# Kernel optimization log

Hardware: AMD Instinct MI355X
Metric: run time of the kernel (lower is better)

The kernel has to match this reference:

```python
import jax, jax.numpy as jnp
import numpy as np

EPS = 1e-6
D = 512      # embedding_dim
M = 4        # n_modules
B = 4        # batch
S = 128      # seq_len
K = 32       # stack_size
STEPS = 16   # max_steps (ACT)
SCALE = D ** (-0.5)


def _clin(zr, zi, Wr, Wi, sub):
    # complex linear: (Wr + i Wi)(zr + i zi), torch Linear convention y = x @ W.T
    yr = jnp.einsum(sub, zr, Wr) - jnp.einsum(sub, zi, Wi)
    yi = jnp.einsum(sub, zi, Wr) + jnp.einsum(sub, zr, Wi)
    return yr, yi


def forward_fn(x_real, x_imag, Wl_r, Wl_i, Wq_r, Wq_i, Wk_r, Wk_i, Wv_r, Wv_i,
               ln_scale, ln_shift, mod_bias, gate_mask,
               score_w, score_b, conf_w, conf_b, halt_w, halt_b,
               ctrl_w, ctrl_b, st_score_w, st_score_b, st_conf_w, st_conf_b):
    mem0 = jnp.zeros((B, K, 2 * D), x_real.dtype)
    ptr0 = jnp.zeros((B, K), x_real.dtype).at[:, 0].set(1.0)
    acc0 = jnp.zeros((B, S, 2 * D), x_real.dtype)
    rem0 = jnp.ones((B,), x_real.dtype)

    def step(carry, _):
        sr, si, mem, ptr, acc, rem = carry
        # ComplexAttentionBlock (all M modules vectorized on axis m)
        cr = 0.5 * x_real + 0.5 * sr
        ci = 0.5 * x_imag + 0.5 * si
        zr, zi = _clin(cr, ci, Wl_r, Wl_i, 'bsd,mod->bmso')   # [B,M,S,D]
        # ComplexLayerNorm (magnitude LN, unbiased var as torch.var default)
        mag = jnp.sqrt(zr * zr + zi * zi) + EPS
        mean = mag.mean(-1, keepdims=True)
        var = mag.var(-1, keepdims=True, ddof=1)
        nm = (mag - mean) / jnp.sqrt(var + EPS)
        nm = nm * ln_scale[None, :, None, :] + ln_shift[None, :, None, :]
        ph = jnp.arctan2(zi, zr)
        zr = nm * jnp.cos(ph)
        zi = nm * jnp.sin(ph)
        # ModReLU
        nrm = jnp.sqrt(zr * zr + zi * zi) + EPS
        sc = jax.nn.relu(nrm + mod_bias[None, :, None, :]) / nrm
        zr = zr * sc
        zi = zi * sc
        # ComplexAttention over concatenated real/imag q,k
        sub = 'bmsd,mod->bmso'
        qr, qi = _clin(zr, zi, Wq_r, Wq_i, sub)
        kr, ki = _clin(zr, zi, Wk_r, Wk_i, sub)
        vr, vi = _clin(zr, zi, Wv_r, Wv_i, sub)
        qf = jnp.concatenate([qr, qi], -1)   # [B,M,S,2D]
        kf = jnp.concatenate([kr, ki], -1)
        attn = jax.nn.softmax(jnp.einsum('bmse,bmte->bmst', qf, kf) * SCALE, axis=-1)
        ar = jnp.einsum('bmst,bmtd->bmsd', attn, vr)
        ai = jnp.einsum('bmst,bmtd->bmsd', attn, vi)
        # SigmoidGatingMask
        g = jax.nn.sigmoid(gate_mask)[None, :, None, :]
        pr = ar * g
        pi = ai * g
        flat = jnp.concatenate([pr, pi], -1)  # [B,M,S,2D]
        score = jnp.einsum('bmse,me->bms', flat, score_w) + score_b[None, :, None]
        conf = jax.nn.sigmoid(jnp.einsum('bmse,me->bms', flat, conf_w) + conf_b[None, :, None])
        halt = jnp.einsum('bmse,me->bms', flat, halt_w) + halt_b[None, :, None]
        # DifferentiableStack on seq-pooled broadcast state
        flat_in = jnp.concatenate([sr.mean(1), si.mean(1)], -1)  # [B,2D]
        control = jax.nn.softmax(flat_in @ ctrl_w + ctrl_b, axis=-1)  # [B,3]
        push, pop, noop = control[:, 0:1], control[:, 1:2], control[:, 2:3]
        ptr_up = jnp.roll(ptr, 1, axis=1)
        ptr_dn = jnp.roll(ptr, -1, axis=1)
        new_ptr = push * ptr_up + pop * ptr_dn + noop * ptr
        new_ptr = new_ptr / (new_ptr.sum(1, keepdims=True) + EPS)
        wmask = push * ptr_up                                   # [B,K]
        new_mem = wmask[..., None] * flat_in[:, None, :] + mem * (1.0 - wmask[..., None])
        read = (new_mem * new_ptr[..., None]).sum(1)            # [B,2D]
        sp_r, sp_i = read[:, :D], read[:, D:]
        st_sc = read @ st_score_w + st_score_b[0]               # [B]
        st_cf = jax.nn.sigmoid(read @ st_conf_w + st_conf_b[0])
        # combine M block proposals + stack proposal via score*confidence softmax
        all_pr = jnp.concatenate([pr, jnp.broadcast_to(sp_r[:, None, None, :], (B, 1, S, D))], 1)
        all_pi = jnp.concatenate([pi, jnp.broadcast_to(sp_i[:, None, None, :], (B, 1, S, D))], 1)
        all_sc = jnp.concatenate([score, jnp.broadcast_to(st_sc[:, None, None], (B, 1, S))], 1)
        all_cf = jnp.concatenate([conf, jnp.broadcast_to(st_cf[:, None, None], (B, 1, S))], 1)
        w = jax.nn.softmax(all_sc * all_cf, axis=1)[..., None]  # [B,M+1,S,1]
        new_sr = (w * all_pr).sum(1)
        new_si = (w * all_pi).sum(1)
        # ACT halting accumulation
        p = jax.nn.sigmoid(halt).mean(axis=(1, 2))              # [B]
        acc = acc + (p * rem)[:, None, None] * jnp.concatenate([new_sr, new_si], -1)
        rem = rem * (1.0 - p)
        return (new_sr, new_si, new_mem, new_ptr, acc, rem), None

    carry, _ = jax.lax.scan(step, (x_real, x_imag, mem0, ptr0, acc0, rem0), None, length=STEPS)
    sr, si, _, _, acc, rem = carry
    # add ACT remainder weight on final state
    out = acc + rem[:, None, None] * jnp.concatenate([sr, si], -1)
    return out  # [B,S,2D] real/imag concat


def setup_inputs() -> dict:
    key = jax.random.key(0)
    ks = jax.random.split(key, 24)
    w = 1.0 / np.sqrt(D)
    h = 0.02
    inp = {
        'x_real': jax.random.normal(ks[0], (B, S, D), jnp.float32),
        'x_imag': jax.random.normal(ks[1], (B, S, D), jnp.float32),
        'Wl_r': jax.random.normal(ks[2], (M, D, D), jnp.float32) * w,
        'Wl_i': jax.random.normal(ks[3], (M, D, D), jnp.float32) * w,
        'Wq_r': jax.random.normal(ks[4], (M, D, D), jnp.float32) * w,
        'Wq_i': jax.random.normal(ks[5], (M, D, D), jnp.float32) * w,
        'Wk_r': jax.random.normal(ks[6], (M, D, D), jnp.float32) * w,
        'Wk_i': jax.random.normal(ks[7], (M, D, D), jnp.float32) * w,
        'Wv_r': jax.random.normal(ks[8], (M, D, D), jnp.float32) * w,
        'Wv_i': jax.random.normal(ks[9], (M, D, D), jnp.float32) * w,
        'ln_scale': jnp.ones((M, D), jnp.float32),
        'ln_shift': jnp.zeros((M, D), jnp.float32),
        'mod_bias': jnp.zeros((M, D), jnp.float32),
        'gate_mask': jnp.ones((M, D), jnp.float32),
        'score_w': jax.random.normal(ks[10], (M, 2 * D), jnp.float32) * h,
        'score_b': jnp.zeros((M,), jnp.float32),
        'conf_w': jax.random.normal(ks[11], (M, 2 * D), jnp.float32) * h,
        'conf_b': jnp.zeros((M,), jnp.float32),
        'halt_w': jax.random.normal(ks[12], (M, 2 * D), jnp.float32) * h,
        'halt_b': jnp.full((M,), -4.0, jnp.float32),  # nn.init.constant_(halt_head.bias, -4.0)
        'ctrl_w': jax.random.normal(ks[13], (2 * D, 3), jnp.float32) * h,
        'ctrl_b': jnp.zeros((3,), jnp.float32),
        'st_score_w': jax.random.normal(ks[14], (2 * D,), jnp.float32) * h,
        'st_score_b': jnp.zeros((1,), jnp.float32),
        'st_conf_w': jax.random.normal(ks[15], (2 * D,), jnp.float32) * h,
        'st_conf_b': jnp.zeros((1,), jnp.float32),
    }
    return inp


def reference(x_real, x_imag, Wl_r, Wl_i, Wq_r, Wq_i, Wk_r, Wk_i, Wv_r, Wv_i,
              ln_scale, ln_shift, mod_bias, gate_mask,
              score_w, score_b, conf_w, conf_b, halt_w, halt_b,
              ctrl_w, ctrl_b, st_score_w, st_score_b, st_conf_w, st_conf_b):
    return forward_fn(x_real, x_imag, Wl_r, Wl_i, Wq_r, Wq_i, Wk_r, Wk_i, Wv_r, Wv_i,
                      ln_scale, ln_shift, mod_bias, gate_mask,
                      score_w, score_b, conf_w, conf_b, halt_w, halt_b,
                      ctrl_w, ctrl_b, st_score_w, st_score_b, st_conf_w, st_conf_b)
```

## Files before the change

kernel.cpp:

```cpp
#include <hip/hip_runtime.h>

#define DD 512
#define MM 4
#define BB 4
#define SS 128
#define KK 32
#define NSTEPS 16
#define EPSF 1e-6f
#define SCALEF 0.04419417382415922f

typedef unsigned short u16;
typedef __bf16 bf16x8 __attribute__((ext_vector_type(8)));
typedef u16 u16x8 __attribute__((ext_vector_type(8)));
typedef float f32x16 __attribute__((ext_vector_type(16)));

__device__ inline void split_bf16(float x, u16& h, u16& l) {
  __bf16 hb = (__bf16)x;
  float hf = (float)hb;
  __bf16 lb = (__bf16)(x - hf);
  h = __builtin_bit_cast(u16, hb);
  l = __builtin_bit_cast(u16, lb);
}

__global__ void k_convw(const float* __restrict__ src, u16* __restrict__ dst) {
  int idx = blockIdx.x * 256 + threadIdx.x;
  int row = idx >> 9, k = idx & 511;
  u16 h, l;
  split_bf16(src[idx], h, l);
  dst[(size_t)row * 1024 + k] = h;
  dst[(size_t)row * 1024 + 512 + k] = l;
}

__global__ void k_init(const float* __restrict__ xr, const float* __restrict__ xi,
                       float* __restrict__ sr, float* __restrict__ si,
                       float* __restrict__ acc, float* __restrict__ memv,
                       float* __restrict__ ptrv, float* __restrict__ rem,
                       u16* __restrict__ crbf, u16* __restrict__ cibf) {
  int idx = blockIdx.x * 256 + threadIdx.x;
  if (idx < BB * SS * 2 * DD) acc[idx] = 0.f;
  if (idx < BB * SS * DD) {
    float a = xr[idx], b = xi[idx];
    sr[idx] = a; si[idx] = b;
    int row = idx >> 9, d = idx & 511;
    u16 h, l;
    split_bf16(a, h, l);
    crbf[(size_t)row * 1024 + d] = h;
    crbf[(size_t)row * 1024 + 512 + d] = l;
    split_bf16(b, h, l);
    cibf[(size_t)row * 1024 + d] = h;
    cibf[(size_t)row * 1024 + 512 + d] = l;
  }
  if (idx < BB * KK * 2 * DD) memv[idx] = 0.f;
  if (idx < BB * KK) ptrv[idx] = ((idx & (KK - 1)) == 0) ? 1.f : 0.f;
  if (idx < BB) rem[idx] = 1.f;
}

__global__ void k_flatctrl(const float* __restrict__ sr, const float* __restrict__ si,
                           const float* __restrict__ ctrl_w, const float* __restrict__ ctrl_b,
                           float* __restrict__ ptrv, float* __restrict__ flat_in,
                           float* __restrict__ nptrg, float* __restrict__ wmg,
                           float* __restrict__ stacc) {
  int b = blockIdx.x;
  int tid = threadIdx.x;
  __shared__ float red[3 * 256];
  __shared__ float ctrl[3], optr[KK], nptr_s[KK], wm_s[KK], normf;

  if (tid < KK) optr[tid] = ptrv[b * KK + tid];

  int e4 = tid * 4;
  const float* basep = (e4 < DD) ? sr : si;
  int d4 = (e4 < DD) ? e4 : (e4 - DD);
  float4 accv = make_float4(0.f, 0.f, 0.f, 0.f);
  size_t base = (size_t)b * SS * DD + d4;
  for (int s = 0; s < SS; s++) {
    float4 v = *(const float4*)&basep[base + (size_t)s * DD];
    accv.x += v.x; accv.y += v.y; accv.z += v.z; accv.w += v.w;
  }
  accv.x *= (1.0f / SS); accv.y *= (1.0f / SS); accv.z *= (1.0f / SS); accv.w *= (1.0f / SS);
  *(float4*)&flat_in[b * 2 * DD + e4] = accv;
  float fv[4] = {accv.x, accv.y, accv.z, accv.w};
  float d0 = 0.f, d1 = 0.f, d2 = 0.f;
#pragma unroll
  for (int j = 0; j < 4; j++) {
    d0 += fv[j] * ctrl_w[(e4 + j) * 3 + 0];
    d1 += fv[j] * ctrl_w[(e4 + j) * 3 + 1];
    d2 += fv[j] * ctrl_w[(e4 + j) * 3 + 2];
  }
  red[tid] = d0; red[256 + tid] = d1; red[512 + tid] = d2;
  __syncthreads();
  for (int off = 128; off > 0; off >>= 1) {
    if (tid < off) {
      red[tid] += red[tid + off];
      red[256 + tid] += red[256 + tid + off];
      red[512 + tid] += red[512 + tid + off];
    }
    __syncthreads();
  }
  if (tid == 0) {
    float l0 = red[0] + ctrl_b[0], l1 = red[256] + ctrl_b[1], l2 = red[512] + ctrl_b[2];
    float mx = fmaxf(l0, fmaxf(l1, l2));
    float e0 = expf(l0 - mx), e1 = expf(l1 - mx), e2 = expf(l2 - mx);
    float s = e0 + e1 + e2;
    ctrl[0] = e0 / s; ctrl[1] = e1 / s; ctrl[2] = e2 / s;
    stacc[b * 2] = 0.f; stacc[b * 2 + 1] = 0.f;
  }
  __syncthreads();
  if (tid < KK) {
    float up = optr[(tid + KK - 1) & (KK - 1)];
    float dn = optr[(tid + 1) & (KK - 1)];
    float cu = optr[tid];
    nptr_s[tid] = ctrl[0] * up + ctrl[1] * dn + ctrl[2] * cu;
    wm_s[tid] = ctrl[0] * up;
  }
  __syncthreads();
  if (tid == 0) {
    float s = 0.f;
    for (int k = 0; k < KK; k++) s += nptr_s[k];
    normf = 1.f / (s + EPSF);
  }
  __syncthreads();
  if (tid < KK) {
    float np = nptr_s[tid] * normf;
    ptrv[b * KK + tid] = np;
    nptrg[b * KK + tid] = np;
    wmg[b * KK + tid] = wm_s[tid];
  }
}

#define LSTR 72

__global__ __launch_bounds__(256) void k_gemm_mfma(
    const u16* __restrict__ Ar, const u16* __restrict__ Ai,
    const u16* __restrict__ Wr, const u16* __restrict__ Wi,
    float* __restrict__ Cr, float* __restrict__ Ci) {
  __shared__ u16 sAr[64][LSTR], sAi[64][LSTR], sWr[64][LSTR], sWi[64][LSTR];
  int m = blockIdx.z;
  int row_blk = blockIdx.y * 64, o_blk = blockIdx.x * 64;
  int tid = threadIdx.x;

  int lrow = tid >> 3, lk8 = (tid & 7) << 3;
  size_t arow0 = (size_t)(row_blk + lrow), arow1 = arow0 + 32;
  size_t wrow0 = (size_t)m * DD + o_blk + lrow, wrow1 = wrow0 + 32;

  int wave = tid >> 6, lane = tid & 63;
  int wrow = (wave >> 1) * 32, wcol = (wave & 1) * 32;
  int l31 = lane & 31, khalf = (lane >> 5) * 8;

  f32x16 accP, accN, accI;
  for (int i = 0; i < 16; i++) { accP[i] = 0.f; accN[i] = 0.f; accI[i] = 0.f; }

  u16x8 g0 = *(const u16x8*)&Ar[arow0 * 1024 + lk8];
  u16x8 g1 = *(const u16x8*)&Ar[arow1 * 1024 + lk8];
  u16x8 g2 = *(const u16x8*)&Ai[arow0 * 1024 + lk8];
  u16x8 g3 = *(const u16x8*)&Ai[arow1 * 1024 + lk8];
  u16x8 g4 = *(const u16x8*)&Wr[wrow0 * 1024 + lk8];
  u16x8 g5 = *(const u16x8*)&Wr[wrow1 * 1024 + lk8];
  u16x8 g6 = *(const u16x8*)&Wi[wrow0 * 1024 + lk8];
  u16x8 g7 = *(const u16x8*)&Wi[wrow1 * 1024 + lk8];

  for (int it = 0; it < 24; ++it) {
    __syncthreads();
    *(u16x8*)&sAr[lrow][lk8] = g0;
    *(u16x8*)&sAr[lrow + 32][lk8] = g1;
    *(u16x8*)&sAi[lrow][lk8] = g2;
    *(u16x8*)&sAi[lrow + 32][lk8] = g3;
    *(u16x8*)&sWr[lrow][lk8] = g4;
    *(u16x8*)&sWr[lrow + 32][lk8] = g5;
    *(u16x8*)&sWi[lrow][lk8] = g6;
    *(u16x8*)&sWi[lrow + 32][lk8] = g7;
    u16x8 n0, n1, n2, n3, n4, n5, n6, n7;
    if (it < 23) {
      int it2 = it + 1, seg = it2 >> 3, k0 = (it2 & 7) * 64;
      int aofs = (seg == 1) ? 512 : 0, wofs = (seg == 2) ? 512 : 0;
      n0 = *(const u16x8*)&Ar[arow0 * 1024 + aofs + k0 + lk8];
      n1 = *(const u16x8*)&Ar[arow1 * 1024 + aofs + k0 + lk8];
      n2 = *(const u16x8*)&Ai[arow0 * 1024 + aofs + k0 + lk8];
      n3 = *(const u16x8*)&Ai[arow1 * 1024 + aofs + k0 + lk8];
      n4 = *(const u16x8*)&Wr[wrow0 * 1024 + wofs + k0 + lk8];
      n5 = *(const u16x8*)&Wr[wrow1 * 1024 + wofs + k0 + lk8];
      n6 = *(const u16x8*)&Wi[wrow0 * 1024 + wofs + k0 + lk8];
      n7 = *(const u16x8*)&Wi[wrow1 * 1024 + wofs + k0 + lk8];
    }
    __syncthreads();
#pragma unroll
    for (int kk = 0; kk < 64; kk += 16) {
      bf16x8 fAr = *(const bf16x8*)&sAr[wrow + l31][kk + khalf];
      bf16x8 fAi = *(const bf16x8*)&sAi[wrow + l31][kk + khalf];
      bf16x8 fWr = *(const bf16x8*)&sWr[wcol + l31][kk + khalf];
      bf16x8 fWi = *(const bf16x8*)&sWi[wcol + l31][kk + khalf];
      accP = __builtin_amdgcn_mfma_f32_32x32x16_bf16(fAr, fWr, accP, 0, 0, 0);
      accN = __builtin_amdgcn_mfma_f32_32x32x16_bf16(fAi, fWi, accN, 0, 0, 0);
      accI = __builtin_amdgcn_mfma_f32_32x32x16_bf16(fAi, fWr, accI, 0, 0, 0);
      accI = __builtin_amdgcn_mfma_f32_32x32x16_bf16(fAr, fWi, accI, 0, 0, 0);
    }
    if (it < 23) {
      g0 = n0; g1 = n1; g2 = n2; g3 = n3; g4 = n4; g5 = n5; g6 = n6; g7 = n7;
    }
  }

  int o = o_blk + wcol + l31;
#pragma unroll
  for (int reg = 0; reg < 16; reg++) {
    int r_in = (reg & 3) + 8 * (reg >> 2) + 4 * (lane >> 5);
    int gr = row_blk + wrow + r_in;
    int b = gr >> 7, s = gr & (SS - 1);
    size_t crow = (size_t)((b * MM + m) * SS + s);
    Cr[crow * DD + o] = accP[reg] - accN[reg];
    Ci[crow * DD + o] = accI[reg];
  }
}

__global__ __launch_bounds__(256) void k_gemm_qkv(
    const u16* __restrict__ Ar, const u16* __restrict__ Ai,
    const u16* __restrict__ wbf, size_t WSLOT,
    u16* __restrict__ qbr, u16* __restrict__ qbi,
    u16* __restrict__ kbr, u16* __restrict__ kbi,
    u16* __restrict__ vbr, u16* __restrict__ vbi) {
  __shared__ u16 sAr[64][LSTR], sAi[64][LSTR], sWr[64][LSTR], sWi[64][LSTR];
  int zid = blockIdx.z;
  int m = zid / 3, w = zid - 3 * m;
  const u16* Wr = wbf + (size_t)(2 + 2 * w) * WSLOT;
  const u16* Wi = Wr + WSLOT;
  int row_blk = blockIdx.y * 64, o_blk = blockIdx.x * 64;
  int tid = threadIdx.x;

  int lrow = tid >> 3, lk8 = (tid & 7) << 3;
  int gr0 = row_blk + lrow, gr1 = gr0 + 32;
  size_t arow0 = (size_t)(((gr0 >> 7) * MM + m) * SS + (gr0 & (SS - 1)));
  size_t arow1 = (size_t)(((gr1 >> 7) * MM + m) * SS + (gr1 & (SS - 1)));
  size_t wrow0 = (size_t)m * DD + o_blk + lrow, wrow1 = wrow0 + 32;

  int wave = tid >> 6, lane = tid & 63;
  int wrow = (wave >> 1) * 32, wcol = (wave & 1) * 32;
  int l31 = lane & 31, khalf = (lane >> 5) * 8;

  f32x16 accP, accN, accI;
  for (int i = 0; i < 16; i++) { accP[i] = 0.f; accN[i] = 0.f; accI[i] = 0.f; }

  u16x8 g0 = *(const u16x8*)&Ar[arow0 * 1024 + lk8];
  u16x8 g1 = *(const u16x8*)&Ar[arow1 * 1024 + lk8];
  u16x8 g2 = *(const u16x8*)&Ai[arow0 * 1024 + lk8];
  u16x8 g3 = *(const u16x8*)&Ai[arow1 * 1024 + lk8];
  u16x8 g4 = *(const u16x8*)&Wr[wrow0 * 1024 + lk8];
  u16x8 g5 = *(const u16x8*)&Wr[wrow1 * 1024 + lk8];
  u16x8 g6 = *(const u16x8*)&Wi[wrow0 * 1024 + lk8];
  u16x8 g7 = *(const u16x8*)&Wi[wrow1 * 1024 + lk8];

  for (int it = 0; it < 24; ++it) {
    __syncthreads();
    *(u16x8*)&sAr[lrow][lk8] = g0;
    *(u16x8*)&sAr[lrow + 32][lk8] = g1;
    *(u16x8*)&sAi[lrow][lk8] = g2;
    *(u16x8*)&sAi[lrow + 32][lk8] = g3;
    *(u16x8*)&sWr[lrow][lk8] = g4;
    *(u16x8*)&sWr[lrow + 32][lk8] = g5;
    *(u16x8*)&sWi[lrow][lk8] = g6;
    *(u16x8*)&sWi[lrow + 32][lk8] = g7;
    u16x8 n0, n1, n2, n3, n4, n5, n6, n7;
    if (it < 23) {
      int it2 = it + 1, seg = it2 >> 3, k0 = (it2 & 7) * 64;
      int aofs = (seg == 1) ? 512 : 0, wofs = (seg == 2) ? 512 : 0;
      n0 = *(const u16x8*)&Ar[arow0 * 1024 + aofs + k0 + lk8];
      n1 = *(const u16x8*)&Ar[arow1 * 1024 + aofs + k0 + lk8];
      n2 = *(const u16x8*)&Ai[arow0 * 1024 + aofs + k0 + lk8];
      n3 = *(const u16x8*)&Ai[arow1 * 1024 + aofs + k0 + lk8];
      n4 = *(const u16x8*)&Wr[wrow0 * 1024 + wofs + k0 + lk8];
      n5 = *(const u16x8*)&Wr[wrow1 * 1024 + wofs + k0 + lk8];
      n6 = *(const u16x8*)&Wi[wrow0 * 1024 + wofs + k0 + lk8];
      n7 = *(const u16x8*)&Wi[wrow1 * 1024 + wofs + k0 + lk8];
    }
    __syncthreads();
#pragma unroll
    for (int kk = 0; kk < 64; kk += 16) {
      bf16x8 fAr = *(const bf16x8*)&sAr[wrow + l31][kk + khalf];
      bf16x8 fAi = *(const bf16x8*)&sAi[wrow + l31][kk + khalf];
      bf16x8 fWr = *(const bf16x8*)&sWr[wcol + l31][kk + khalf];
      bf16x8 fWi = *(const bf16x8*)&sWi[wcol + l31][kk + khalf];
      accP = __builtin_amdgcn_mfma_f32_32x32x16_bf16(fAr, fWr, accP, 0, 0, 0);
      accN = __builtin_amdgcn_mfma_f32_32x32x16_bf16(fAi, fWi, accN, 0, 0, 0);
      accI = __builtin_amdgcn_mfma_f32_32x32x16_bf16(fAi, fWr, accI, 0, 0, 0);
      accI = __builtin_amdgcn_mfma_f32_32x32x16_bf16(fAr, fWi, accI, 0, 0, 0);
    }
    if (it < 23) {
      g0 = n0; g1 = n1; g2 = n2; g3 = n3; g4 = n4; g5 = n5; g6 = n6; g7 = n7;
    }
  }

  u16* Cr = (w == 0) ? qbr : ((w == 1) ? kbr : vbr);
  u16* Ci = (w == 0) ? qbi : ((w == 1) ? kbi : vbi);
  int o = o_blk + wcol + l31;
#pragma unroll
  for (int reg = 0; reg < 16; reg++) {
    int r_in = (reg & 3) + 8 * (reg >> 2) + 4 * (lane >> 5);
    int gr = row_blk + wrow + r_in;
    int b = gr >> 7, s = gr & (SS - 1);
    size_t crow = (size_t)((b * MM + m) * SS + s);
    u16 h, l;
    split_bf16(accP[reg] - accN[reg], h, l);
    Cr[crow * 1024 + o] = h;
    Cr[crow * 1024 + 512 + o] = l;
    split_bf16(accI[reg], h, l);
    Ci[crow * 1024 + o] = h;
    Ci[crow * 1024 + 512 + o] = l;
  }
}

__global__ __launch_bounds__(256) void k_scores_sm(
    const u16* __restrict__ Q_r, const u16* __restrict__ Q_i,
    const u16* __restrict__ K_r, const u16* __restrict__ K_i,
    u16* __restrict__ Pb) {
  __shared__ __align__(16) char smem[55296];
  u16 (*sQr)[LSTR] = (u16(*)[LSTR])smem;
  u16 (*sQi)[LSTR] = (u16(*)[LSTR])(smem + 9216);
  u16 (*sKr)[LSTR] = (u16(*)[LSTR])(smem + 18432);
  u16 (*sKi)[LSTR] = (u16(*)[LSTR])(smem + 36864);
  float (*stile)[132] = (float(*)[132])smem;

  int bm = blockIdx.z;
  int s_blk = blockIdx.y * 64;
  int tid = threadIdx.x;
  int lrow = tid >> 3, lk8 = (tid & 7) << 3;
  size_t qrow0 = (size_t)(bm * SS + s_blk + lrow), qrow1 = qrow0 + 32;
  size_t krow = (size_t)(bm * SS + lrow);

  int wave = tid >> 6, lane = tid & 63;
  int srow_w = (wave & 1) * 32;
  int tcol_w = (wave >> 1) * 64;
  int l31 = lane & 31, khalf = (lane >> 5) * 8;

  f32x16 acc0, acc1;
  for (int i = 0; i < 16; i++) { acc0[i] = 0.f; acc1[i] = 0.f; }

  for (int it = 0; it < 24; ++it) {
    int seg = it >> 3, k0 = (it & 7) * 64;
    int qofs = (seg == 1) ? 512 : 0;
    int kofs = (seg == 2) ? 512 : 0;
    u16x8 q0 = *(const u16x8*)&Q_r[qrow0 * 1024 + qofs + k0 + lk8];
    u16x8 q1 = *(const u16x8*)&Q_r[qrow1 * 1024 + qofs + k0 + lk8];
    u16x8 q2 = *(const u16x8*)&Q_i[qrow0 * 1024 + qofs + k0 + lk8];
    u16x8 q3 = *(const u16x8*)&Q_i[qrow1 * 1024 + qofs + k0 + lk8];
    u16x8 kr0 = *(const u16x8*)&K_r[(krow + 0) * 1024 + kofs + k0 + lk8];
    u16x8 kr1 = *(const u16x8*)&K_r[(krow + 32) * 1024 + kofs + k0 + lk8];
    u16x8 kr2 = *(const u16x8*)&K_r[(krow + 64) * 1024 + kofs + k0 + lk8];
    u16x8 kr3 = *(const u16x8*)&K_r[(krow + 96) * 1024 + kofs + k0 + lk8];
    u16x8 ki0 = *(const u16x8*)&K_i[(krow + 0) * 1024 + kofs + k0 + lk8];
    u16x8 ki1 = *(const u16x8*)&K_i[(krow + 32) * 1024 + kofs + k0 + lk8];
    u16x8 ki2 = *(const u16x8*)&K_i[(krow + 64) * 1024 + kofs + k0 + lk8];
    u16x8 ki3 = *(const u16x8*)&K_i[(krow + 96) * 1024 + kofs + k0 + lk8];
    __syncthreads();
    *(u16x8*)&sQr[lrow][lk8] = q0;
    *(u16x8*)&sQr[lrow + 32][lk8] = q1;
    *(u16x8*)&sQi[lrow][lk8] = q2;
    *(u16x8*)&sQi[lrow + 32][lk8] = q3;
    *(u16x8*)&sKr[lrow][lk8] = kr0;
    *(u16x8*)&sKr[lrow + 32][lk8] = kr1;
    *(u16x8*)&sKr[lrow + 64][lk8] = kr2;
    *(u16x8*)&sKr[lrow + 96][lk8] = kr3;
    *(u16x8*)&sKi[lrow][lk8] = ki0;
    *(u16x8*)&sKi[lrow + 32][lk8] = ki1;
    *(u16x8*)&sKi[lrow + 64][lk8] = ki2;
    *(u16x8*)&sKi[lrow + 96][lk8] = ki3;
    __syncthreads();
#pragma unroll
    for (int kk = 0; kk < 64; kk += 16) {
      bf16x8 fQr = *(const bf16x8*)&sQr[srow_w + l31][kk + khalf];
      bf16x8 fQi = *(const bf16x8*)&sQi[srow_w + l31][kk + khalf];
      bf16x8 fKr0 = *(const bf16x8*)&sKr[tcol_w + l31][kk + khalf];
      bf16x8 fKr1 = *(const bf16x8*)&sKr[tcol_w + 32 + l31][kk + khalf];
      bf16x8 fKi0 = *(const bf16x8*)&sKi[tcol_w + l31][kk + khalf];
      bf16x8 fKi1 = *(const bf16x8*)&sKi[tcol_w + 32 + l31][kk + khalf];
      acc0 = __builtin_amdgcn_mfma_f32_32x32x16_bf16(fQr, fKr0, acc0, 0, 0, 0);
      acc0 = __builtin_amdgcn_mfma_f32_32x32x16_bf16(fQi, fKi0, acc0, 0, 0, 0);
      acc1 = __builtin_amdgcn_mfma_f32_32x32x16_bf16(fQr, fKr1, acc1, 0, 0, 0);
      acc1 = __builtin_amdgcn_mfma_f32_32x32x16_bf16(fQi, fKi1, acc1, 0, 0, 0);
    }
  }

  __syncthreads();
#pragma unroll
  for (int reg = 0; reg < 16; reg++) {
    int r = srow_w + (reg & 3) + 8 * (reg >> 2) + 4 * (lane >> 5);
    stile[r][tcol_w + l31] = acc0[reg] * SCALEF;
    stile[r][tcol_w + 32 + l31] = acc1[reg] * SCALEF;
  }
  __syncthreads();
  int row = tid >> 2;
  int quarter = tid & 3;
  float mx = -3.4e38f;
#pragma unroll
  for (int j = 0; j < 32; j++) mx = fmaxf(mx, stile[row][quarter * 32 + j]);
  mx = fmaxf(mx, __shfl_xor(mx, 1));
  mx = fmaxf(mx, __shfl_xor(mx, 2));
  float ev[32];
  float sum = 0.f;
#pragma unroll
  for (int j = 0; j < 32; j++) {
    ev[j] = expf(stile[row][quarter * 32 + j] - mx);
    sum += ev[j];
  }
  sum += __shfl_xor(sum, 1);
  sum += __shfl_xor(sum, 2);
  float inv = 1.f / sum;
  size_t prow = (size_t)(bm * SS + s_blk + row) * 256;
#pragma unroll
  for (int j = 0; j < 32; j++) {
    int c = quarter * 32 + j;
    u16 h, l;
    split_bf16(ev[j] * inv, h, l);
    Pb[prow + c] = h;
    Pb[prow + 128 + c] = l;
  }
}

__global__ __launch_bounds__(256) void k_pv(
    const u16* __restrict__ Pb, const u16* __restrict__ vbr, const u16* __restrict__ vbi,
    const float* __restrict__ gate_mask,
    float* __restrict__ pr, float* __restrict__ pi) {
  __shared__ u16 sP[64][LSTR], sVr[64][LSTR], sVi[64][LSTR];
  int bm = blockIdx.z;
  int m = bm & (MM - 1);
  int s_blk = blockIdx.y * 64;
  int o_blk = blockIdx.x * 64;
  int tid = threadIdx.x;
  int lrow = tid >> 3, lk8 = (tid & 7) << 3;
  size_t prow0 = (size_t)(bm * SS + s_blk + lrow), prow1 = prow0 + 32;

  int wave = tid >> 6, lane = tid & 63;
  int wrow = (wave >> 1) * 32;
  int wcol = (wave & 1) * 32;
  int l31 = lane & 31, khalf = (lane >> 5) * 8;

  f32x16 accR, accI;
  for (int i = 0; i < 16; i++) { accR[i] = 0.f; accI[i] = 0.f; }

  for (int it = 0; it < 6; ++it) {
    int seg = it >> 1, k0 = (it & 1) * 64;
    int pofs = (seg == 1) ? 128 : 0;
    int vofs = (seg == 2) ? 512 : 0;
    u16x8 p0 = *(const u16x8*)&Pb[prow0 * 256 + pofs + k0 + lk8];
    u16x8 p1 = *(const u16x8*)&Pb[prow1 * 256 + pofs + k0 + lk8];
    size_t vrow0 = (size_t)(bm * SS + k0 + lrow), vrow1 = vrow0 + 32;
    u16x8 v0 = *(const u16x8*)&vbr[vrow0 * 1024 + vofs + o_blk + lk8];
    u16x8 v1 = *(const u16x8*)&vbr[vrow1 * 1024 + vofs + o_blk + lk8];
    u16x8 w0 = *(const u16x8*)&vbi[vrow0 * 1024 + vofs + o_blk + lk8];
    u16x8 w1 = *(const u16x8*)&vbi[vrow1 * 1024 + vofs + o_blk + lk8];
    __syncthreads();
    *(u16x8*)&sP[lrow][lk8] = p0;
    *(u16x8*)&sP[lrow + 32][lk8] = p1;
    *(u16x8*)&sVr[lrow][lk8] = v0;
    *(u16x8*)&sVr[lrow + 32][lk8] = v1;
    *(u16x8*)&sVi[lrow][lk8] = w0;
    *(u16x8*)&sVi[lrow + 32][lk8] = w1;
    __syncthreads();
#pragma unroll
    for (int kk = 0; kk < 64; kk += 16) {
      bf16x8 fP = *(const bf16x8*)&sP[wrow + l31][kk + khalf];
      u16x8 ar, ai;
#pragma unroll
      for (int j = 0; j < 8; j++) {
        ar[j] = sVr[kk + khalf + j][wcol + l31];
        ai[j] = sVi[kk + khalf + j][wcol + l31];
      }
      accR = __builtin_amdgcn_mfma_f32_32x32x16_bf16(fP, __builtin_bit_cast(bf16x8, ar), accR, 0, 0, 0);
      accI = __builtin_amdgcn_mfma_f32_32x32x16_bf16(fP, __builtin_bit_cast(bf16x8, ai), accI, 0, 0, 0);
    }
  }

  int d = o_blk + wcol + l31;
  float g = 1.f / (1.f + expf(-gate_mask[m * DD + d]));
#pragma unroll
  for (int reg = 0; reg < 16; reg++) {
    int r_in = (reg & 3) + 8 * (reg >> 2) + 4 * (lane >> 5);
    size_t crow = (size_t)(bm * SS + s_blk + wrow + r_in);
    pr[crow * DD + d] = accR[reg] * g;
    pi[crow * DD + d] = accI[reg] * g;
  }
}

__global__ void k_heads(const float* __restrict__ pr, const float* __restrict__ pi,
                        const float* __restrict__ score_w, const float* __restrict__ score_b,
                        const float* __restrict__ conf_w, const float* __restrict__ conf_b,
                        const float* __restrict__ halt_w, const float* __restrict__ halt_b,
                        float* __restrict__ score, float* __restrict__ conf,
                        float* __restrict__ halt) {
  int row = blockIdx.x;
  int m = (row >> 7) & (MM - 1);
  int tid = threadIdx.x;
  __shared__ float r0[256], r1[256], r2[256];
  float sp = 0.f, cp = 0.f, hp = 0.f;
#pragma unroll
  for (int i = 0; i < 4; i++) {
    int e = tid + i * 256;
    float v = (e < DD) ? pr[(size_t)row * DD + e] : pi[(size_t)row * DD + e - DD];
    sp += v * score_w[m * 2 * DD + e];
    cp += v * conf_w[m * 2 * DD + e];
    hp += v * halt_w[m * 2 * DD + e];
  }
  r0[tid] = sp; r1[tid] = cp; r2[tid] = hp;
  __syncthreads();
  for (int off = 128; off > 0; off >>= 1) {
    if (tid < off) { r0[tid] += r0[tid + off]; r1[tid] += r1[tid + off]; r2[tid] += r2[tid + off]; }
    __syncthreads();
  }
  if (tid == 0) {
    score[row] = r0[0] + score_b[m];
    conf[row] = 1.f / (1.f + expf(-(r1[0] + conf_b[m])));
    halt[row] = r2[0] + halt_b[m];
  }
}

__global__ void k_lnphase(const float* __restrict__ zr, const float* __restrict__ zi,
                          const float* __restrict__ ln_scale, const float* __restrict__ ln_shift,
                          const float* __restrict__ mod_bias,
                          u16* __restrict__ zbr, u16* __restrict__ zbi) {
  int row = blockIdx.x;
  int m = (row >> 7) & (MM - 1);
  int tid = threadIdx.x;
  size_t base = (size_t)row * DD;
  float zrv[4], ziv[4], rv[4];
  float sum = 0.f, sumsq = 0.f;
#pragma unroll
  for (int i = 0; i < 4; i++) {
    int o = tid + i * 128;
    float a = zr[base + o], bv = zi[base + o];
    zrv[i] = a; ziv[i] = bv;
    float r = sqrtf(a * a + bv * bv);
    rv[i] = r;
    float mg = r + EPSF;
    sum += mg;
    sumsq += mg * mg;
  }
  __shared__ float rs[128], rq[128];
  rs[tid] = sum; rq[tid] = sumsq;
  __syncthreads();
  for (int off = 64; off > 0; off >>= 1) {
    if (tid < off) { rs[tid] += rs[tid + off]; rq[tid] += rq[tid + off]; }
    __syncthreads();
  }
  float mean = rs[0] * (1.0f / DD);
  float var = (rq[0] - (float)DD * mean * mean) * (1.0f / (DD - 1));
  float inv = 1.0f / sqrtf(var + EPSF);
#pragma unroll
  for (int i = 0; i < 4; i++) {
    int o = tid + i * 128;
    float mg = rv[i] + EPSF;
    float nm = (mg - mean) * inv * ln_scale[m * DD + o] + ln_shift[m * DD + o];
    float r = rv[i];
    float cosp, sinp;
    if (r > 0.f) { cosp = zrv[i] / r; sinp = ziv[i] / r; }
    else { cosp = 1.f; sinp = 0.f; }
    float z1r = nm * cosp, z1i = nm * sinp;
    float nrm = sqrtf(z1r * z1r + z1i * z1i) + EPSF;
    float sc = fmaxf(nrm + mod_bias[m * DD + o], 0.f) / nrm;
    u16 h, l;
    split_bf16(z1r * sc, h, l);
    zbr[(size_t)row * 1024 + o] = h;
    zbr[(size_t)row * 1024 + 512 + o] = l;
    split_bf16(z1i * sc, h, l);
    zbi[(size_t)row * 1024 + o] = h;
    zbi[(size_t)row * 1024 + 512 + o] = l;
  }
}

__global__ void k_memup(const float* __restrict__ flat_in,
                        const float* __restrict__ nptrg, const float* __restrict__ wmg,
                        float* __restrict__ memv, float* __restrict__ readv,
                        const float* __restrict__ st_score_w, const float* __restrict__ st_conf_w,
                        float* __restrict__ stacc) {
  int b = blockIdx.x >> 2;
  int chunk = blockIdx.x & 3;
  int tid = threadIdx.x;
  int e = chunk * 256 + tid;
  __shared__ float nptr[KK], wm[KK];
  __shared__ float red[256], red2[256];
  if (tid < KK) { nptr[tid] = nptrg[b * KK + tid]; wm[tid] = wmg[b * KK + tid]; }
  __syncthreads();
  float fl = flat_in[b * 2 * DD + e];
  float racc = 0.f;
#pragma unroll
  for (int k = 0; k < KK; k++) {
    size_t idx = ((size_t)(b * KK + k)) * 2 * DD + e;
    float nm = wm[k] * fl + memv[idx] * (1.f - wm[k]);
    memv[idx] = nm;
    racc += nm * nptr[k];
  }
  readv[b * 2 * DD + e] = racc;
  red[tid] = racc * st_score_w[e];
  red2[tid] = racc * st_conf_w[e];
  __syncthreads();
  for (int off = 128; off > 0; off >>= 1) {
    if (tid < off) { red[tid] += red[tid + off]; red2[tid] += red2[tid + off]; }
    __syncthreads();
  }
  if (tid == 0) {
    atomicAdd(&stacc[b * 2], red[0]);
    atomicAdd(&stacc[b * 2 + 1], red2[0]);
  }
}

__global__ void k_haltp(const float* __restrict__ halt, float* __restrict__ rem,
                        float* __restrict__ coeff, const float* __restrict__ stacc,
                        const float* __restrict__ st_score_b, const float* __restrict__ st_conf_b,
                        float* __restrict__ stv) {
  int b = blockIdx.x;
  int tid = threadIdx.x;
  __shared__ float red[256];
  float v0 = halt[b * MM * SS + tid];
  float v1 = halt[b * MM * SS + 256 + tid];
  red[tid] = 1.f / (1.f + expf(-v0)) + 1.f / (1.f + expf(-v1));
  __syncthreads();
  for (int off = 128; off > 0; off >>= 1) {
    if (tid < off) red[tid] += red[tid + off];
    __syncthreads();
  }
  if (tid == 0) {
    float p = red[0] * (1.0f / (MM * SS));
    float r = rem[b];
    coeff[b] = p * r;
    rem[b] = r * (1.f - p);
    stv[b] = stacc[b * 2] + st_score_b[0];
    stv[BB + b] = 1.f / (1.f + expf(-(stacc[b * 2 + 1] + st_conf_b[0])));
  }
}

__global__ void k_combine(const float* __restrict__ pr, const float* __restrict__ pi,
                          const float* __restrict__ score, const float* __restrict__ conf,
                          const float* __restrict__ stv, const float* __restrict__ readv,
                          const float* __restrict__ coeff,
                          const float* __restrict__ xr, const float* __restrict__ xi,
                          float* __restrict__ sr, float* __restrict__ si, float* __restrict__ acc,
                          u16* __restrict__ crbf, u16* __restrict__ cibf) {
  int bs = blockIdx.x;
  int b = bs >> 7, s = bs & (SS - 1);
  int tid = threadIdx.x;
  __shared__ float w[5];
  if (tid == 0) {
    float l[5];
    for (int m = 0; m < MM; m++) {
      int r = (b * MM + m) * SS + s;
      l[m] = score[r] * conf[r];
    }
    l[4] = stv[b] * stv[BB + b];
    float mx = l[0];
    for (int j = 1; j < 5; j++) mx = fmaxf(mx, l[j]);
    float sum = 0.f;
    for (int j = 0; j < 5; j++) { l[j] = expf(l[j] - mx); sum += l[j]; }
    for (int j = 0; j < 5; j++) w[j] = l[j] / sum;
  }
  __syncthreads();
  float cf = coeff[b];
#pragma unroll
  for (int i = 0; i < 2; i++) {
    int d = tid + i * 256;
    float nsr = w[4] * readv[b * 2 * DD + d];
    float nsi = w[4] * readv[b * 2 * DD + DD + d];
#pragma unroll
    for (int m = 0; m < MM; m++) {
      size_t off = ((size_t)((b * MM + m) * SS + s)) * DD + d;
      nsr += w[m] * pr[off];
      nsi += w[m] * pi[off];
    }
    size_t sidx = (size_t)bs * DD + d;
    sr[sidx] = nsr;
    si[sidx] = nsi;
    size_t aoff = (size_t)bs * 2 * DD;
    acc[aoff + d] += cf * nsr;
    acc[aoff + DD + d] += cf * nsi;
    u16 h, l;
    split_bf16(0.5f * xr[sidx] + 0.5f * nsr, h, l);
    crbf[(size_t)bs * 1024 + d] = h;
    crbf[(size_t)bs * 1024 + 512 + d] = l;
    split_bf16(0.5f * xi[sidx] + 0.5f * nsi, h, l);
    cibf[(size_t)bs * 1024 + d] = h;
    cibf[(size_t)bs * 1024 + 512 + d] = l;
  }
}

__global__ void k_final(const float* __restrict__ acc, const float* __restrict__ rem,
                        const float* __restrict__ sr, const float* __restrict__ si,
                        float* __restrict__ out) {
  int idx = blockIdx.x * 256 + threadIdx.x;
  int e = idx & (2 * DD - 1);
  int bs = idx >> 10;
  int b = bs >> 7;
  float v = (e < DD) ? sr[(size_t)bs * DD + e] : si[(size_t)bs * DD + e - DD];
  out[idx] = acc[idx] + rem[b] * v;
}

extern "C" void kernel_launch(void* const* d_in, const int* in_sizes, int n_in,
                              void* d_out, int out_size, void* d_ws, size_t ws_size,
                              hipStream_t stream) {
  const float* xr = (const float*)d_in[0];
  const float* xi = (const float*)d_in[1];
  const float* Wl_r = (const float*)d_in[2];
  const float* Wl_i = (const float*)d_in[3];
  const float* Wq_r = (const float*)d_in[4];
  const float* Wq_i = (const float*)d_in[5];
  const float* Wk_r = (const float*)d_in[6];
  const float* Wk_i = (const float*)d_in[7];
  const float* Wv_r = (const float*)d_in[8];
  const float* Wv_i = (const float*)d_in[9];
  const float* ln_scale = (const float*)d_in[10];
  const float* ln_shift = (const float*)d_in[11];
  const float* mod_bias = (const float*)d_in[12];
  const float* gate_mask = (const float*)d_in[13];
  const float* score_w = (const float*)d_in[14];
  const float* score_b = (const float*)d_in[15];
  const float* conf_w = (const float*)d_in[16];
  const float* conf_b = (const float*)d_in[17];
  const float* halt_w = (const float*)d_in[18];
  const float* halt_b = (const float*)d_in[19];
  const float* ctrl_w = (const float*)d_in[20];
  const float* ctrl_b = (const float*)d_in[21];
  const float* st_score_w = (const float*)d_in[22];
  const float* st_score_b = (const float*)d_in[23];
  const float* st_conf_w = (const float*)d_in[24];
  const float* st_conf_b = (const float*)d_in[25];
  float* out = (float*)d_out;

  const int BSD = BB * SS * DD;
  const int BMSD = BB * MM * SS * DD;
  const size_t WSLOT = (size_t)MM * DD * 1024;

  char* pc = (char*)d_ws;
  float* sr = (float*)pc; pc += (size_t)BSD * 4;
  float* si = (float*)pc; pc += (size_t)BSD * 4;
  float* zr = (float*)pc; pc += (size_t)BMSD * 4;
  float* zi = (float*)pc; pc += (size_t)BMSD * 4;
  float* prb = (float*)pc; pc += (size_t)BMSD * 4;
  float* pib = (float*)pc; pc += (size_t)BMSD * 4;
  float* scorev = (float*)pc; pc += (size_t)BB * MM * SS * 4;
  float* confv = (float*)pc; pc += (size_t)BB * MM * SS * 4;
  float* haltv = (float*)pc; pc += (size_t)BB * MM * SS * 4;
  float* flat = (float*)pc; pc += (size_t)BB * 2 * DD * 4;
  float* stacc = (float*)pc; pc += 64;
  float* nptrg = (float*)pc; pc += (size_t)BB * KK * 4;
  float* wmg = (float*)pc; pc += (size_t)BB * KK * 4;
  float* memv = (float*)pc; pc += (size_t)BB * KK * 2 * DD * 4;
  float* ptrv = (float*)pc; pc += (size_t)BB * KK * 4;
  float* readv = (float*)pc; pc += (size_t)BB * 2 * DD * 4;
  float* stv = (float*)pc; pc += (size_t)2 * BB * 4;
  float* accb = (float*)pc; pc += (size_t)BB * SS * 2 * DD * 4;
  float* rem = (float*)pc; pc += (size_t)BB * 4;
  float* coeff = (float*)pc; pc += (size_t)BB * 4;
  u16* crbf = (u16*)pc; pc += (size_t)BB * SS * 1024 * 2;
  u16* cibf = (u16*)pc; pc += (size_t)BB * SS * 1024 * 2;
  u16* zbr = (u16*)pc; pc += (size_t)BB * MM * SS * 1024 * 2;
  u16* zbi = (u16*)pc; pc += (size_t)BB * MM * SS * 1024 * 2;
  u16* qbr = (u16*)pc; pc += (size_t)BB * MM * SS * 1024 * 2;
  u16* qbi = (u16*)pc; pc += (size_t)BB * MM * SS * 1024 * 2;
  u16* kbr = (u16*)pc; pc += (size_t)BB * MM * SS * 1024 * 2;
  u16* kbi = (u16*)pc; pc += (size_t)BB * MM * SS * 1024 * 2;
  u16* vbr = (u16*)pc; pc += (size_t)BB * MM * SS * 1024 * 2;
  u16* vbi = (u16*)pc; pc += (size_t)BB * MM * SS * 1024 * 2;
  u16* Pb  = (u16*)pc; pc += (size_t)BB * MM * SS * 256 * 2;
  u16* wbf = (u16*)pc; pc += 8 * WSLOT * 2;

  k_convw<<<4096, 256, 0, stream>>>(Wl_r, wbf + 0 * WSLOT);
  k_convw<<<4096, 256, 0, stream>>>(Wl_i, wbf + 1 * WSLOT);
  k_convw<<<4096, 256, 0, stream>>>(Wq_r, wbf + 2 * WSLOT);
  k_convw<<<4096, 256, 0, stream>>>(Wq_i, wbf + 3 * WSLOT);
  k_convw<<<4096, 256, 0, stream>>>(Wk_r, wbf + 4 * WSLOT);
  k_convw<<<4096, 256, 0, stream>>>(Wk_i, wbf + 5 * WSLOT);
  k_convw<<<4096, 256, 0, stream>>>(Wv_r, wbf + 6 * WSLOT);
  k_convw<<<4096, 256, 0, stream>>>(Wv_i, wbf + 7 * WSLOT);

  k_init<<<2048, 256, 0, stream>>>(xr, xi, sr, si, accb, memv, ptrv, rem, crbf, cibf);

  dim3 ggrid(DD / 64, (BB * SS) / 64, MM);
  dim3 qgrid(DD / 64, (BB * SS) / 64, MM * 3);
  dim3 smgrid(1, SS / 64, BB * MM);
  dim3 pvgrid(DD / 64, SS / 64, BB * MM);

  for (int step = 0; step < NSTEPS; ++step) {
    k_flatctrl<<<BB, 256, 0, stream>>>(sr, si, ctrl_w, ctrl_b, ptrv, flat, nptrg, wmg, stacc);
    k_gemm_mfma<<<ggrid, 256, 0, stream>>>(crbf, cibf, wbf + 0 * WSLOT, wbf + 1 * WSLOT, zr, zi);
    k_lnphase<<<BB * MM * SS, 128, 0, stream>>>(zr, zi, ln_scale, ln_shift, mod_bias, zbr, zbi);
    k_gemm_qkv<<<qgrid, 256, 0, stream>>>(zbr, zbi, wbf, WSLOT, qbr, qbi, kbr, kbi, vbr, vbi);
    k_scores_sm<<<smgrid, 256, 0, stream>>>(qbr, qbi, kbr, kbi, Pb);
    k_pv<<<pvgrid, 256, 0, stream>>>(Pb, vbr, vbi, gate_mask, prb, pib);
    k_heads<<<BB * MM * SS, 256, 0, stream>>>(prb, pib, score_w, score_b, conf_w, conf_b,
                                              halt_w, halt_b, scorev, confv, haltv);
    k_memup<<<BB * 4, 256, 0, stream>>>(flat, nptrg, wmg, memv, readv,
                                        st_score_w, st_conf_w, stacc);
    k_haltp<<<BB, 256, 0, stream>>>(haltv, rem, coeff, stacc, st_score_b, st_conf_b, stv);
    k_combine<<<BB * SS, 256, 0, stream>>>(prb, pib, scorev, confv, stv, readv, coeff,
                                           xr, xi, sr, si, accb, crbf, cibf);
  }

  k_final<<<(BB * SS * 2 * DD) / 256, 256, 0, stream>>>(accb, rem, sr, si, out);
}
```

Measured before the change: 2.397 ms.

## Fuse head projections into PV epilogue, merge halting into memup, retile scores softmax

Folds the score, confidence and halt projections into the k_pv epilogue with wave shuffles, shared-memory atomics and global atomics, which removes the k_heads launch and its full reread of the pr/pi tensors. Halting probability and remainder updates move into k_memup using ping-pong remainder buffers, and the stack score and confidence sigmoid moves into k_combine, which removes the k_haltp launch. k_scores_sm now processes 32 query rows per block instead of 64, doubling the block count to raise occupancy. The register prefetch in both GEMMs is replaced by loads issued in the same iteration. The atomics make summation order nondeterministic, and the GEMMs lose their load/compute overlap.

```diff
diff --git a/kernel.cpp b/kernel.cpp
--- a/kernel.cpp
+++ b/kernel.cpp
@@ -59,11 +59,18 @@
                            const float* __restrict__ ctrl_w, const float* __restrict__ ctrl_b,
                            float* __restrict__ ptrv, float* __restrict__ flat_in,
                            float* __restrict__ nptrg, float* __restrict__ wmg,
-                           float* __restrict__ stacc) {
+                           float* __restrict__ stacc,
+                           float* __restrict__ scorev, float* __restrict__ confv,
+                           float* __restrict__ haltacc) {
   int b = blockIdx.x;
   int tid = threadIdx.x;
   __shared__ float red[3 * 256];
   __shared__ float ctrl[3], optr[KK], nptr_s[KK], wm_s[KK], normf;
+
+  int zid = b * 256 + tid;
+  scorev[zid] = 0.f; scorev[zid + 1024] = 0.f;
+  confv[zid] = 0.f; confv[zid + 1024] = 0.f;
+  haltacc[zid] = 0.f; haltacc[zid + 1024] = 0.f;
 
   if (tid < KK) optr[tid] = ptrv[b * KK + tid];
 
@@ -149,16 +156,17 @@
   f32x16 accP, accN, accI;
   for (int i = 0; i < 16; i++) { accP[i] = 0.f; accN[i] = 0.f; accI[i] = 0.f; }
 
-  u16x8 g0 = *(const u16x8*)&Ar[arow0 * 1024 + lk8];
-  u16x8 g1 = *(const u16x8*)&Ar[arow1 * 1024 + lk8];
-  u16x8 g2 = *(const u16x8*)&Ai[arow0 * 1024 + lk8];
-  u16x8 g3 = *(const u16x8*)&Ai[arow1 * 1024 + lk8];
-  u16x8 g4 = *(const u16x8*)&Wr[wrow0 * 1024 + lk8];
-  u16x8 g5 = *(const u16x8*)&Wr[wrow1 * 1024 + lk8];
-  u16x8 g6 = *(const u16x8*)&Wi[wrow0 * 1024 + lk8];
-  u16x8 g7 = *(const u16x8*)&Wi[wrow1 * 1024 + lk8];
-
   for (int it = 0; it < 24; ++it) {
+    int seg = it >> 3, k0 = (it & 7) * 64;
+    int aofs = (seg == 1) ? 512 : 0, wofs = (seg == 2) ? 512 : 0;
+    u16x8 g0 = *(const u16x8*)&Ar[arow0 * 1024 + aofs + k0 + lk8];
+    u16x8 g1 = *(const u16x8*)&Ar[arow1 * 1024 + aofs + k0 + lk8];
+    u16x8 g2 = *(const u16x8*)&Ai[arow0 * 1024 + aofs + k0 + lk8];
+    u16x8 g3 = *(const u16x8*)&Ai[arow1 * 1024 + aofs + k0 + lk8];
+    u16x8 g4 = *(const u16x8*)&Wr[wrow0 * 1024 + wofs + k0 + lk8];
+    u16x8 g5 = *(const u16x8*)&Wr[wrow1 * 1024 + wofs + k0 + lk8];
+    u16x8 g6 = *(const u16x8*)&Wi[wrow0 * 1024 + wofs + k0 + lk8];
+    u16x8 g7 = *(const u16x8*)&Wi[wrow1 * 1024 + wofs + k0 + lk8];
     __syncthreads();
     *(u16x8*)&sAr[lrow][lk8] = g0;
     *(u16x8*)&sAr[lrow + 32][lk8] = g1;
@@ -168,19 +176,6 @@
     *(u16x8*)&sWr[lrow + 32][lk8] = g5;
     *(u16x8*)&sWi[lrow][lk8] = g6;
     *(u16x8*)&sWi[lrow + 32][lk8] = g7;
-    u16x8 n0, n1, n2, n3, n4, n5, n6, n7;
-    if (it < 23) {
-      int it2 = it + 1, seg = it2 >> 3, k0 = (it2 & 7) * 64;
-      int aofs = (seg == 1) ? 512 : 0, wofs = (seg == 2) ? 512 : 0;
-      n0 = *(const u16x8*)&Ar[arow0 * 1024 + aofs + k0 + lk8];
-      n1 = *(const u16x8*)&Ar[arow1 * 1024 + aofs + k0 + lk8];
-      n2 = *(const u16x8*)&Ai[arow0 * 1024 + aofs + k0 + lk8];
-      n3 = *(const u16x8*)&Ai[arow1 * 1024 + aofs + k0 + lk8];
-      n4 = *(const u16x8*)&Wr[wrow0 * 1024 + wofs + k0 + lk8];
-      n5 = *(const u16x8*)&Wr[wrow1 * 1024 + wofs + k0 + lk8];
-      n6 = *(const u16x8*)&Wi[wrow0 * 1024 + wofs + k0 + lk8];
-      n7 = *(const u16x8*)&Wi[wrow1 * 1024 + wofs + k0 + lk8];
-    }
     __syncthreads();
 #pragma unroll
     for (int kk = 0; kk < 64; kk += 16) {
@@ -192,9 +187,6 @@
       accN = __builtin_amdgcn_mfma_f32_32x32x16_bf16(fAi, fWi, accN, 0, 0, 0);
       accI = __builtin_amdgcn_mfma_f32_32x32x16_bf16(fAi, fWr, accI, 0, 0, 0);
       accI = __builtin_amdgcn_mfma_f32_32x32x16_bf16(fAr, fWi, accI, 0, 0, 0);
-    }
-    if (it < 23) {
-      g0 = n0; g1 = n1; g2 = n2; g3 = n3; g4 = n4; g5 = n5; g6 = n6; g7 = n7;
     }
   }
 
@@ -237,16 +229,17 @@
   f32x16 accP, accN, accI;
   for (int i = 0; i < 16; i++) { accP[i] = 0.f; accN[i] = 0.f; accI[i] = 0.f; }
 
-  u16x8 g0 = *(const u16x8*)&Ar[arow0 * 1024 + lk8];
-  u16x8 g1 = *(const u16x8*)&Ar[arow1 * 1024 + lk8];
-  u16x8 g2 = *(const u16x8*)&Ai[arow0 * 1024 + lk8];
-  u16x8 g3 = *(const u16x8*)&Ai[arow1 * 1024 + lk8];
-  u16x8 g4 = *(const u16x8*)&Wr[wrow0 * 1024 + lk8];
-  u16x8 g5 = *(const u16x8*)&Wr[wrow1 * 1024 + lk8];
-  u16x8 g6 = *(const u16x8*)&Wi[wrow0 * 1024 + lk8];
-  u16x8 g7 = *(const u16x8*)&Wi[wrow1 * 1024 + lk8];
-
   for (int it = 0; it < 24; ++it) {
+    int seg = it >> 3, k0 = (it & 7) * 64;
+    int aofs = (seg == 1) ? 512 : 0, wofs = (seg == 2) ? 512 : 0;
+    u16x8 g0 = *(const u16x8*)&Ar[arow0 * 1024 + aofs + k0 + lk8];
+    u16x8 g1 = *(const u16x8*)&Ar[arow1 * 1024 + aofs + k0 + lk8];
+    u16x8 g2 = *(const u16x8*)&Ai[arow0 * 1024 + aofs + k0 + lk8];
+    u16x8 g3 = *(const u16x8*)&Ai[arow1 * 1024 + aofs + k0 + lk8];
+    u16x8 g4 = *(const u16x8*)&Wr[wrow0 * 1024 + wofs + k0 + lk8];
+    u16x8 g5 = *(const u16x8*)&Wr[wrow1 * 1024 + wofs + k0 + lk8];
+    u16x8 g6 = *(const u16x8*)&Wi[wrow0 * 1024 + wofs + k0 + lk8];
+    u16x8 g7 = *(const u16x8*)&Wi[wrow1 * 1024 + wofs + k0 + lk8];
     __syncthreads();
     *(u16x8*)&sAr[lrow][lk8] = g0;
     *(u16x8*)&sAr[lrow + 32][lk8] = g1;
@@ -256,19 +249,6 @@
     *(u16x8*)&sWr[lrow + 32][lk8] = g5;
     *(u16x8*)&sWi[lrow][lk8] = g6;
     *(u16x8*)&sWi[lrow + 32][lk8] = g7;
-    u16x8 n0, n1, n2, n3, n4, n5, n6, n7;
-    if (it < 23) {
-      int it2 = it + 1, seg = it2 >> 3, k0 = (it2 & 7) * 64;
-      int aofs = (seg == 1) ? 512 : 0, wofs = (seg == 2) ? 512 : 0;
-      n0 = *(const u16x8*)&Ar[arow0 * 1024 + aofs + k0 + lk8];
-      n1 = *(const u16x8*)&Ar[arow1 * 1024 + aofs + k0 + lk8];
-      n2 = *(const u16x8*)&Ai[arow0 * 1024 + aofs + k0 + lk8];
-      n3 = *(const u16x8*)&Ai[arow1 * 1024 + aofs + k0 + lk8];
-      n4 = *(const u16x8*)&Wr[wrow0 * 1024 + wofs + k0 + lk8];
-      n5 = *(const u16x8*)&Wr[wrow1 * 1024 + wofs + k0 + lk8];
-      n6 = *(const u16x8*)&Wi[wrow0 * 1024 + wofs + k0 + lk8];
-      n7 = *(const u16x8*)&Wi[wrow1 * 1024 + wofs + k0 + lk8];
-    }
     __syncthreads();
 #pragma unroll
     for (int kk = 0; kk < 64; kk += 16) {
@@ -280,9 +260,6 @@
       accN = __builtin_amdgcn_mfma_f32_32x32x16_bf16(fAi, fWi, accN, 0, 0, 0);
       accI = __builtin_amdgcn_mfma_f32_32x32x16_bf16(fAi, fWr, accI, 0, 0, 0);
       accI = __builtin_amdgcn_mfma_f32_32x32x16_bf16(fAr, fWi, accI, 0, 0, 0);
-    }
-    if (it < 23) {
-      g0 = n0; g1 = n1; g2 = n2; g3 = n3; g4 = n4; g5 = n5; g6 = n6; g7 = n7;
     }
   }
 
@@ -309,36 +286,33 @@
     const u16* __restrict__ Q_r, const u16* __restrict__ Q_i,
     const u16* __restrict__ K_r, const u16* __restrict__ K_i,
     u16* __restrict__ Pb) {
-  __shared__ __align__(16) char smem[55296];
+  __shared__ __align__(16) char smem[46080];
   u16 (*sQr)[LSTR] = (u16(*)[LSTR])smem;
-  u16 (*sQi)[LSTR] = (u16(*)[LSTR])(smem + 9216);
-  u16 (*sKr)[LSTR] = (u16(*)[LSTR])(smem + 18432);
-  u16 (*sKi)[LSTR] = (u16(*)[LSTR])(smem + 36864);
+  u16 (*sQi)[LSTR] = (u16(*)[LSTR])(smem + 4608);
+  u16 (*sKr)[LSTR] = (u16(*)[LSTR])(smem + 9216);
+  u16 (*sKi)[LSTR] = (u16(*)[LSTR])(smem + 27648);
   float (*stile)[132] = (float(*)[132])smem;
 
   int bm = blockIdx.z;
-  int s_blk = blockIdx.y * 64;
+  int s_blk = blockIdx.y * 32;
   int tid = threadIdx.x;
   int lrow = tid >> 3, lk8 = (tid & 7) << 3;
-  size_t qrow0 = (size_t)(bm * SS + s_blk + lrow), qrow1 = qrow0 + 32;
+  size_t qrow = (size_t)(bm * SS + s_blk + lrow);
   size_t krow = (size_t)(bm * SS + lrow);
 
   int wave = tid >> 6, lane = tid & 63;
-  int srow_w = (wave & 1) * 32;
-  int tcol_w = (wave >> 1) * 64;
+  int tcol_w = wave * 32;
   int l31 = lane & 31, khalf = (lane >> 5) * 8;
 
-  f32x16 acc0, acc1;
-  for (int i = 0; i < 16; i++) { acc0[i] = 0.f; acc1[i] = 0.f; }
+  f32x16 acc;
+  for (int i = 0; i < 16; i++) acc[i] = 0.f;
 
   for (int it = 0; it < 24; ++it) {
     int seg = it >> 3, k0 = (it & 7) * 64;
     int qofs = (seg == 1) ? 512 : 0;
     int kofs = (seg == 2) ? 512 : 0;
-    u16x8 q0 = *(const u16x8*)&Q_r[qrow0 * 1024 + qofs + k0 + lk8];
-    u16x8 q1 = *(const u16x8*)&Q_r[qrow1 * 1024 + qofs + k0 + lk8];
-    u16x8 q2 = *(const u16x8*)&Q_i[qrow0 * 1024 + qofs + k0 + lk8];
-    u16x8 q3 = *(const u16x8*)&Q_i[qrow1 * 1024 + qofs + k0 + lk8];
+    u16x8 q0 = *(const u16x8*)&Q_r[qrow * 1024 + qofs + k0 + lk8];
+    u16x8 q1 = *(const u16x8*)&Q_i[qrow * 1024 + qofs + k0 + lk8];
     u16x8 kr0 = *(const u16x8*)&K_r[(krow + 0) * 1024 + kofs + k0 + lk8];
     u16x8 kr1 = *(const u16x8*)&K_r[(krow + 32) * 1024 + kofs + k0 + lk8];
     u16x8 kr2 = *(const u16x8*)&K_r[(krow + 64) * 1024 + kofs + k0 + lk8];
@@ -349,9 +323,7 @@
     u16x8 ki3 = *(const u16x8*)&K_i[(krow + 96) * 1024 + kofs + k0 + lk8];
     __syncthreads();
     *(u16x8*)&sQr[lrow][lk8] = q0;
-    *(u16x8*)&sQr[lrow + 32][lk8] = q1;
-    *(u16x8*)&sQi[lrow][lk8] = q2;
-    *(u16x8*)&sQi[lrow + 32][lk8] = q3;
+    *(u16x8*)&sQi[lrow][lk8] = q1;
     *(u16x8*)&sKr[lrow][lk8] = kr0;
     *(u16x8*)&sKr[lrow + 32][lk8] = kr1;
     *(u16x8*)&sKr[lrow + 64][lk8] = kr2;
@@ -363,48 +335,45 @@
     __syncthreads();
 #pragma unroll
     for (int kk = 0; kk < 64; kk += 16) {
-      bf16x8 fQr = *(const bf16x8*)&sQr[srow_w + l31][kk + khalf];
-      bf16x8 fQi = *(const bf16x8*)&sQi[srow_w + l31][kk + khalf];
-      bf16x8 fKr0 = *(const bf16x8*)&sKr[tcol_w + l31][kk + khalf];
-      bf16x8 fKr1 = *(const bf16x8*)&sKr[tcol_w + 32 + l31][kk + khalf];
-      bf16x8 fKi0 = *(const bf16x8*)&sKi[tcol_w + l31][kk + khalf];
-      bf16x8 fKi1 = *(const bf16x8*)&sKi[tcol_w + 32 + l31][kk + khalf];
-      acc0 = __builtin_amdgcn_mfma_f32_32x32x16_bf16(fQr, fKr0, acc0, 0, 0, 0);
-      acc0 = __builtin_amdgcn_mfma_f32_32x32x16_bf16(fQi, fKi0, acc0, 0, 0, 0);
-      acc1 = __builtin_amdgcn_mfma_f32_32x32x16_bf16(fQr, fKr1, acc1, 0, 0, 0);
-      acc1 = __builtin_amdgcn_mfma_f32_32x32x16_bf16(fQi, fKi1, acc1, 0, 0, 0);
+      bf16x8 fQr = *(const bf16x8*)&sQr[l31][kk + khalf];
+      bf16x8 fQi = *(const bf16x8*)&sQi[l31][kk + khalf];
+      bf16x8 fKr = *(const bf16x8*)&sKr[tcol_w + l31][kk + khalf];
+      bf16x8 fKi = *(const bf16x8*)&sKi[tcol_w + l31][kk + khalf];
+      acc = __builtin_amdgcn_mfma_f32_32x32x16_bf16(fQr, fKr, acc, 0, 0, 0);
+      acc = __builtin_amdgcn_mfma_f32_32x32x16_bf16(fQi, fKi, acc, 0, 0, 0);
     }
   }
 
   __syncthreads();
 #pragma unroll
   for (int reg = 0; reg < 16; reg++) {
-    int r = srow_w + (reg & 3) + 8 * (reg >> 2) + 4 * (lane >> 5);
-    stile[r][tcol_w + l31] = acc0[reg] * SCALEF;
-    stile[r][tcol_w + 32 + l31] = acc1[reg] * SCALEF;
-  }
-  __syncthreads();
-  int row = tid >> 2;
-  int quarter = tid & 3;
+    int r = (reg & 3) + 8 * (reg >> 2) + 4 * (lane >> 5);
+    stile[r][tcol_w + l31] = acc[reg] * SCALEF;
+  }
+  __syncthreads();
+  int row = tid >> 3;
+  int oct = tid & 7;
   float mx = -3.4e38f;
 #pragma unroll
-  for (int j = 0; j < 32; j++) mx = fmaxf(mx, stile[row][quarter * 32 + j]);
+  for (int j = 0; j < 16; j++) mx = fmaxf(mx, stile[row][oct * 16 + j]);
   mx = fmaxf(mx, __shfl_xor(mx, 1));
   mx = fmaxf(mx, __shfl_xor(mx, 2));
-  float ev[32];
+  mx = fmaxf(mx, __shfl_xor(mx, 4));
+  float ev[16];
   float sum = 0.f;
 #pragma unroll
-  for (int j = 0; j < 32; j++) {
-    ev[j] = expf(stile[row][quarter * 32 + j] - mx);
+  for (int j = 0; j < 16; j++) {
+    ev[j] = expf(stile[row][oct * 16 + j] - mx);
     sum += ev[j];
   }
   sum += __shfl_xor(sum, 1);
   sum += __shfl_xor(sum, 2);
+  sum += __shfl_xor(sum, 4);
   float inv = 1.f / sum;
   size_t prow = (size_t)(bm * SS + s_blk + row) * 256;
 #pragma unroll
-  for (int j = 0; j < 32; j++) {
-    int c = quarter * 32 + j;
+  for (int j = 0; j < 16; j++) {
+    int c = oct * 16 + j;
     u16 h, l;
     split_bf16(ev[j] * inv, h, l);
     Pb[prow + c] = h;
@@ -415,8 +384,12 @@
 __global__ __launch_bounds__(256) void k_pv(
     const u16* __restrict__ Pb, const u16* __restrict__ vbr, const u16* __restrict__ vbi,
     const float* __restrict__ gate_mask,
-    float* __restrict__ pr, float* __restrict__ pi) {
+    const float* __restrict__ score_w, const float* __restrict__ conf_w,
+    const float* __restrict__ halt_w,
+    float* __restrict__ pr, float* __restrict__ pi,
+    float* __restrict__ scorev, float* __restrict__ confv, float* __restrict__ haltacc) {
   __shared__ u16 sP[64][LSTR], sVr[64][LSTR], sVi[64][LSTR];
+  __shared__ float rowAcc[64][3];
   int bm = blockIdx.z;
   int m = bm & (MM - 1);
   int s_blk = blockIdx.y * 64;
@@ -429,6 +402,8 @@
   int wrow = (wave >> 1) * 32;
   int wcol = (wave & 1) * 32;
   int l31 = lane & 31, khalf = (lane >> 5) * 8;
+
+  if (tid < 64) { rowAcc[tid][0] = 0.f; rowAcc[tid][1] = 0.f; rowAcc[tid][2] = 0.f; }
 
   f32x16 accR, accI;
   for (int i = 0; i < 16; i++) { accR[i] = 0.f; accI[i] = 0.f; }
@@ -468,44 +443,38 @@
 
   int d = o_blk + wcol + l31;
   float g = 1.f / (1.f + expf(-gate_mask[m * DD + d]));
+  float sw_r = score_w[m * 1024 + d], sw_i = score_w[m * 1024 + 512 + d];
+  float cw_r = conf_w[m * 1024 + d],  cw_i = conf_w[m * 1024 + 512 + d];
+  float hw_r = halt_w[m * 1024 + d],  hw_i = halt_w[m * 1024 + 512 + d];
 #pragma unroll
   for (int reg = 0; reg < 16; reg++) {
     int r_in = (reg & 3) + 8 * (reg >> 2) + 4 * (lane >> 5);
     size_t crow = (size_t)(bm * SS + s_blk + wrow + r_in);
-    pr[crow * DD + d] = accR[reg] * g;
-    pi[crow * DD + d] = accI[reg] * g;
-  }
-}
-
-__global__ void k_heads(const float* __restrict__ pr, const float* __restrict__ pi,
-                        const float* __restrict__ score_w, const float* __restrict__ score_b,
-                        const float* __restrict__ conf_w, const float* __restrict__ conf_b,
-                        const float* __restrict__ halt_w, const float* __restrict__ halt_b,
-                        float* __restrict__ score, float* __restrict__ conf,
-                        float* __restrict__ halt) {
-  int row = blockIdx.x;
-  int m = (row >> 7) & (MM - 1);
-  int tid = threadIdx.x;
-  __shared__ float r0[256], r1[256], r2[256];
-  float sp = 0.f, cp = 0.f, hp = 0.f;
-#pragma unroll
-  for (int i = 0; i < 4; i++) {
-    int e = tid + i * 256;
-    float v = (e < DD) ? pr[(size_t)row * DD + e] : pi[(size_t)row * DD + e - DD];
-    sp += v * score_w[m * 2 * DD + e];
-    cp += v * conf_w[m * 2 * DD + e];
-    hp += v * halt_w[m * 2 * DD + e];
-  }
-  r0[tid] = sp; r1[tid] = cp; r2[tid] = hp;
-  __syncthreads();
-  for (int off = 128; off > 0; off >>= 1) {
-    if (tid < off) { r0[tid] += r0[tid + off]; r1[tid] += r1[tid + off]; r2[tid] += r2[tid + off]; }
-    __syncthreads();
-  }
-  if (tid == 0) {
-    score[row] = r0[0] + score_b[m];
-    conf[row] = 1.f / (1.f + expf(-(r1[0] + conf_b[m])));
-    halt[row] = r2[0] + halt_b[m];
+    float pR = accR[reg] * g, pI = accI[reg] * g;
+    pr[crow * DD + d] = pR;
+    pi[crow * DD + d] = pI;
+    float sp = pR * sw_r + pI * sw_i;
+    float cp = pR * cw_r + pI * cw_i;
+    float hp = pR * hw_r + pI * hw_i;
+#pragma unroll
+    for (int msk = 16; msk >= 1; msk >>= 1) {
+      sp += __shfl_xor(sp, msk);
+      cp += __shfl_xor(cp, msk);
+      hp += __shfl_xor(hp, msk);
+    }
+    if (l31 == 0) {
+      int r = wrow + r_in;
+      atomicAdd(&rowAcc[r][0], sp);
+      atomicAdd(&rowAcc[r][1], cp);
+      atomicAdd(&rowAcc[r][2], hp);
+    }
+  }
+  __syncthreads();
+  if (tid < 64) {
+    size_t rowg = (size_t)(bm * SS + s_blk + tid);
+    atomicAdd(&scorev[rowg], rowAcc[tid][0]);
+    atomicAdd(&confv[rowg], rowAcc[tid][1]);
+    atomicAdd(&haltacc[rowg], rowAcc[tid][2]);
   }
 }
 
@@ -566,14 +535,24 @@
                         const float* __restrict__ nptrg, const float* __restrict__ wmg,
                         float* __restrict__ memv, float* __restrict__ readv,
                         const float* __restrict__ st_score_w, const float* __restrict__ st_conf_w,
-                        float* __restrict__ stacc) {
+                        float* __restrict__ stacc,
+                        const float* __restrict__ haltacc, const float* __restrict__ halt_b,
+                        const float* __restrict__ rem_in, float* __restrict__ rem_out,
+                        float* __restrict__ coeff) {
   int b = blockIdx.x >> 2;
   int chunk = blockIdx.x & 3;
   int tid = threadIdx.x;
   int e = chunk * 256 + tid;
   __shared__ float nptr[KK], wm[KK];
-  __shared__ float red[256], red2[256];
+  __shared__ float red[256], red2[256], red3[256];
   if (tid < KK) { nptr[tid] = nptrg[b * KK + tid]; wm[tid] = wmg[b * KK + tid]; }
+
+  float hsum = 0.f;
+  if (chunk == 0) {
+    float h0 = haltacc[b * 512 + tid] + halt_b[tid >> 7];
+    float h1 = haltacc[b * 512 + 256 + tid] + halt_b[(256 + tid) >> 7];
+    hsum = 1.f / (1.f + expf(-h0)) + 1.f / (1.f + expf(-h1));
+  }
   __syncthreads();
   float fl = flat_in[b * 2 * DD + e];
   float racc = 0.f;
@@ -587,46 +566,30 @@
   readv[b * 2 * DD + e] = racc;
   red[tid] = racc * st_score_w[e];
   red2[tid] = racc * st_conf_w[e];
+  red3[tid] = hsum;
   __syncthreads();
   for (int off = 128; off > 0; off >>= 1) {
-    if (tid < off) { red[tid] += red[tid + off]; red2[tid] += red2[tid + off]; }
+    if (tid < off) { red[tid] += red[tid + off]; red2[tid] += red2[tid + off]; red3[tid] += red3[tid + off]; }
     __syncthreads();
   }
   if (tid == 0) {
     atomicAdd(&stacc[b * 2], red[0]);
     atomicAdd(&stacc[b * 2 + 1], red2[0]);
-  }
-}
-
-__global__ void k_haltp(const float* __restrict__ halt, float* __restrict__ rem,
-                        float* __restrict__ coeff, const float* __restrict__ stacc,
-                        const float* __restrict__ st_score_b, const float* __restrict__ st_conf_b,
-                        float* __restrict__ stv) {
-  int b = blockIdx.x;
-  int tid = threadIdx.x;
-  __shared__ float red[256];
-  float v0 = halt[b * MM * SS + tid];
-  float v1 = halt[b * MM * SS + 256 + tid];
-  red[tid] = 1.f / (1.f + expf(-v0)) + 1.f / (1.f + expf(-v1));
-  __syncthreads();
-  for (int off = 128; off > 0; off >>= 1) {
-    if (tid < off) red[tid] += red[tid + off];
-    __syncthreads();
-  }
-  if (tid == 0) {
-    float p = red[0] * (1.0f / (MM * SS));
-    float r = rem[b];
-    coeff[b] = p * r;
-    rem[b] = r * (1.f - p);
-    stv[b] = stacc[b * 2] + st_score_b[0];
-    stv[BB + b] = 1.f / (1.f + expf(-(stacc[b * 2 + 1] + st_conf_b[0])));
+    if (chunk == 0) {
+      float p = red3[0] * (1.0f / (MM * SS));
+      float r = rem_in[b];
+      coeff[b] = p * r;
+      rem_out[b] = r * (1.f - p);
+    }
   }
 }
 
 __global__ void k_combine(const float* __restrict__ pr, const float* __restrict__ pi,
-                          const float* __restrict__ score, const float* __restrict__ conf,
-                          const float* __restrict__ stv, const float* __restrict__ readv,
-                          const float* __restrict__ coeff,
+                          const float* __restrict__ scorev, const float* __restrict__ confv,
+                          const float* __restrict__ score_b, const float* __restrict__ conf_b,
+                          const float* __restrict__ stacc,
+                          const float* __restrict__ st_score_b, const float* __restrict__ st_conf_b,
+                          const float* __restrict__ readv, const float* __restrict__ coeff,
                           const float* __restrict__ xr, const float* __restrict__ xi,
                           float* __restrict__ sr, float* __restrict__ si, float* __restrict__ acc,
                           u16* __restrict__ crbf, u16* __restrict__ cibf) {
@@ -638,9 +601,13 @@
     float l[5];
     for (int m = 0; m < MM; m++) {
       int r = (b * MM + m) * SS + s;
-      l[m] = score[r] * conf[r];
-    }
-    l[4] = stv[b] * stv[BB + b];
+      float sc = scorev[r] + score_b[m];
+      float cf2 = 1.f / (1.f + expf(-(confv[r] + conf_b[m])));
+      l[m] = sc * cf2;
+    }
+    float sv = stacc[b * 2] + st_score_b[0];
+    float cv = 1.f / (1.f + expf(-(stacc[b * 2 + 1] + st_conf_b[0])));
+    l[4] = sv * cv;
     float mx = l[0];
     for (int j = 1; j < 5; j++) mx = fmaxf(mx, l[j]);
     float sum = 0.f;
@@ -731,7 +698,7 @@
   float* pib = (float*)pc; pc += (size_t)BMSD * 4;
   float* scorev = (float*)pc; pc += (size_t)BB * MM * SS * 4;
   float* confv = (float*)pc; pc += (size_t)BB * MM * SS * 4;
-  float* haltv = (float*)pc; pc += (size_t)BB * MM * SS * 4;
+  float* haltacc = (float*)pc; pc += (size_t)BB * MM * SS * 4;
   float* flat = (float*)pc; pc += (size_t)BB * 2 * DD * 4;
   float* stacc = (float*)pc; pc += 64;
   float* nptrg = (float*)pc; pc += (size_t)BB * KK * 4;
@@ -739,9 +706,9 @@
   float* memv = (float*)pc; pc += (size_t)BB * KK * 2 * DD * 4;
   float* ptrv = (float*)pc; pc += (size_t)BB * KK * 4;
   float* readv = (float*)pc; pc += (size_t)BB * 2 * DD * 4;
-  float* stv = (float*)pc; pc += (size_t)2 * BB * 4;
   float* accb = (float*)pc; pc += (size_t)BB * SS * 2 * DD * 4;
-  float* rem = (float*)pc; pc += (size_t)BB * 4;
+  float* rem0 = (float*)pc; pc += (size_t)BB * 4;
+  float* rem1 = (float*)pc; pc += (size_t)BB * 4;
   float* coeff = (float*)pc; pc += (size_t)BB * 4;
   u16* crbf = (u16*)pc; pc += (size_t)BB * SS * 1024 * 2;
   u16* cibf = (u16*)pc; pc += (size_t)BB * SS * 1024 * 2;
@@ -765,28 +732,31 @@
   k_convw<<<4096, 256, 0, stream>>>(Wv_r, wbf + 6 * WSLOT);
   k_convw<<<4096, 256, 0, stream>>>(Wv_i, wbf + 7 * WSLOT);
 
-  k_init<<<2048, 256, 0, stream>>>(xr, xi, sr, si, accb, memv, ptrv, rem, crbf, cibf);
+  k_init<<<2048, 256, 0, stream>>>(xr, xi, sr, si, accb, memv, ptrv, rem0, crbf, cibf);
 
   dim3 ggrid(DD / 64, (BB * SS) / 64, MM);
   dim3 qgrid(DD / 64, (BB * SS) / 64, MM * 3);
-  dim3 smgrid(1, SS / 64, BB * MM);
+  dim3 smgrid(1, SS / 32, BB * MM);
   dim3 pvgrid(DD / 64, SS / 64, BB * MM);
 
   for (int step = 0; step < NSTEPS; ++step) {
-    k_flatctrl<<<BB, 256, 0, stream>>>(sr, si, ctrl_w, ctrl_b, ptrv, flat, nptrg, wmg, stacc);
+    float* rin = (step & 1) ? rem1 : rem0;
+    float* rout = (step & 1) ? rem0 : rem1;
+    k_flatctrl<<<BB, 256, 0, stream>>>(sr, si, ctrl_w, ctrl_b, ptrv, flat, nptrg, wmg,
+                                       stacc, scorev, confv, haltacc);
     k_gemm_mfma<<<ggrid, 256, 0, stream>>>(crbf, cibf, wbf + 0 * WSLOT, wbf + 1 * WSLOT, zr, zi);
     k_lnphase<<<BB * MM * SS, 128, 0, stream>>>(zr, zi, ln_scale, ln_shift, mod_bias, zbr, zbi);
     k_gemm_qkv<<<qgrid, 256, 0, stream>>>(zbr, zbi, wbf, WSLOT, qbr, qbi, kbr, kbi, vbr, vbi);
     k_scores_sm<<<smgrid, 256, 0, stream>>>(qbr, qbi, kbr, kbi, Pb);
-    k_pv<<<pvgrid, 256, 0, stream>>>(Pb, vbr, vbi, gate_mask, prb, pib);
-    k_heads<<<BB * MM * SS, 256, 0, stream>>>(prb, pib, score_w, score_b, conf_w, conf_b,
-                                              halt_w, halt_b, scorev, confv, haltv);
+    k_pv<<<pvgrid, 256, 0, stream>>>(Pb, vbr, vbi, gate_mask, score_w, conf_w, halt_w,
+                                     prb, pib, scorev, confv, haltacc);
     k_memup<<<BB * 4, 256, 0, stream>>>(flat, nptrg, wmg, memv, readv,
-                                        st_score_w, st_conf_w, stacc);
-    k_haltp<<<BB, 256, 0, stream>>>(haltv, rem, coeff, stacc, st_score_b, st_conf_b, stv);
-    k_combine<<<BB * SS, 256, 0, stream>>>(prb, pib, scorev, confv, stv, readv, coeff,
+                                        st_score_w, st_conf_w, stacc,
+                                        haltacc, halt_b, rin, rout, coeff);
+    k_combine<<<BB * SS, 256, 0, stream>>>(prb, pib, scorev, confv, score_b, conf_b,
+                                           stacc, st_score_b, st_conf_b, readv, coeff,
                                            xr, xi, sr, si, accb, crbf, cibf);
   }
 
-  k_final<<<(BB * SS * 2 * DD) / 256, 256, 0, stream>>>(accb, rem, sr, si, out);
-}
+  k_final<<<(BB * SS * 2 * DD) / 256, 256, 0, stream>>>(accb, rem0, sr, si, out);
+}
```

New measurement: 2.751 ms. 14.8% more time.
